# Performance work log

Hardware: AMD Instinct MI355X
Metric: run time of the kernel (lower is better)

## Reference

```python
import jax, jax.numpy as jnp
import numpy as np

B, S, E, H = 2, 2048, 1024, 16
D = E // H  # head_dim = 64


def _rope_angles(seq_len, d, dtype=jnp.float32):
    # standard RoPE frequencies: theta_i = 10000^{-2i/d}
    inv_freq = 1.0 / (10000.0 ** (jnp.arange(0, d, 2, dtype=dtype) / d))  # [d/2]
    pos = jnp.arange(seq_len, dtype=dtype)                                # [S]
    ang = pos[:, None] * inv_freq[None, :]                                # [S, d/2]
    ang = jnp.concatenate([ang, ang], axis=-1)                            # [S, d]
    return jnp.cos(ang), jnp.sin(ang)


def _rotate_half(t):
    t1, t2 = jnp.split(t, 2, axis=-1)
    return jnp.concatenate([-t2, t1], axis=-1)


def _apply_rope(t, cos, sin):
    # t: [B, H, S, D]; cos/sin: [S, D]
    return t * cos[None, None, :, :] + _rotate_half(t) * sin[None, None, :, :]


def setup_inputs() -> dict:
    key = jax.random.key(0)
    ks = jax.random.split(key, 6)
    x = jax.random.normal(ks[0], (B, S, E), dtype=jnp.float32)
    mask = jnp.tril(jnp.ones((S, S), dtype=bool))  # causal: True = attend
    scale = 1.0 / np.sqrt(E)
    Wq = jax.random.normal(ks[1], (E, E), dtype=jnp.float32) * scale
    Wk = jax.random.normal(ks[2], (E, E), dtype=jnp.float32) * scale
    Wv = jax.random.normal(ks[3], (E, E), dtype=jnp.float32) * scale
    Wo = jax.random.normal(ks[4], (E, E), dtype=jnp.float32) * scale
    z = jnp.zeros((E,), dtype=jnp.float32)
    return {"x": x, "mask": mask, "Wq": Wq, "bq": z, "Wk": Wk, "bk": z,
            "Wv": Wv, "bv": z, "Wo": Wo, "bo": z}


def reference(x, mask, Wq, bq, Wk, bk, Wv, bv, Wo, bo):
    b, s, e = x.shape
    # QKV projections (nn.Linear convention: y = x @ W.T + b)
    def proj(W, bias):
        y = jnp.einsum('bse,fe->bsf', x, W) + bias
        return y.reshape(b, s, H, D).transpose(0, 2, 1, 3)  # [B,H,S,D]
    q, k, v = proj(Wq, bq), proj(Wk, bk), proj(Wv, bv)
    # RoPE on q and k (per-head rotary over head_dim)
    cos, sin = _rope_angles(s, D, dtype=x.dtype)
    q = _apply_rope(q, cos, sin)
    k = _apply_rope(k, cos, sin)
    # SDPA with boolean mask (True = attend)
    scores = jnp.einsum('bhqd,bhkd->bhqk', q, k) / jnp.sqrt(jnp.asarray(D, x.dtype))
    neg = jnp.asarray(jnp.finfo(x.dtype).min, x.dtype)
    scores = jnp.where(mask[None, None, :, :], scores, neg)
    attn = jax.nn.softmax(scores, axis=-1)
    out = jnp.einsum('bhqk,bhkd->bhqd', attn, v)          # [B,H,S,D]
    out = out.transpose(0, 2, 1, 3).reshape(b, s, e)       # [B,S,E]
    return jnp.einsum('bse,fe->bsf', out, Wo) + bo
```

## Files before the change

### kernel.cpp

```cpp
#include <hip/hip_runtime.h>
#include <hip/hip_bf16.h>

typedef unsigned short u16;
typedef unsigned int u32;
typedef __bf16 bf16x8 __attribute__((ext_vector_type(8)));
typedef float f32x4 __attribute__((ext_vector_type(4)));

#define S_LEN 2048
#define NHEAD 16
#define HDIM  64
#define EMB   1024
#define BATCH 2

__device__ __forceinline__ float bf2f(u16 u) {
  union { unsigned int i; float f; } c; c.i = ((unsigned int)u) << 16; return c.f;
}
__device__ __forceinline__ u16 f2bf(float f) {
  union { float f; unsigned int i; } c; c.f = f;
  unsigned int i = c.i;
  return (u16)((i + 0x7FFFu + ((i >> 16) & 1u)) >> 16);
}
__device__ __forceinline__ u16 f2bf_trunc(float f) {
  union { float f; unsigned int i; } c; c.f = f;
  return (u16)(c.i >> 16);
}
__device__ __forceinline__ f32x4 mfma16(bf16x8 a, bf16x8 b, f32x4 c) {
  return __builtin_amdgcn_mfma_f32_16x16x32_bf16(a, b, c, 0, 0, 0);
}
__device__ __forceinline__ void cp16(const u16* g, u16* l) {
  __builtin_amdgcn_global_load_lds(
      (const __attribute__((address_space(1))) u32*)g,
      (__attribute__((address_space(3))) u32*)l, 16, 0, 0);
}

__global__ __launch_bounds__(256) void convert_kernel(
    const void* __restrict__ x, const void* __restrict__ Wq,
    const void* __restrict__ Wk, const void* __restrict__ Wv,
    const void* __restrict__ Wo,
    u16* __restrict__ xb, u16* __restrict__ wqb, u16* __restrict__ wkb,
    u16* __restrict__ wvb, u16* __restrict__ wob,
    int* __restrict__ flag, float2* __restrict__ tab)
{
  __shared__ int s_flag;
  if (threadIdx.x == 0) s_flag = 0;
  __syncthreads();
  {
    const u16* xs = (const u16*)x;
    u16 w0 = xs[threadIdx.x * 2], w1 = xs[threadIdx.x * 2 + 1];
    if ((((w0 >> 7) & 0xFF) >= 0xC0) || (((w1 >> 7) & 0xFF) >= 0xC0))
      atomicOr(&s_flag, 1);
  }
  __syncthreads();
  const int f32io = s_flag;
  if (blockIdx.x == 0 && threadIdx.x == 0) flag[0] = f32io;

  size_t gid = (size_t)blockIdx.x * 256 + threadIdx.x;
  size_t e = gid * 8;
  const void* src; u16* dst; size_t off;
  if (e < 4194304) { src = x; dst = xb; off = e; }
  else {
    size_t rr = e - 4194304;
    int j = (int)(rr >> 20); off = rr & 1048575;
    src = (j == 0) ? Wq : (j == 1) ? Wk : (j == 2) ? Wv : Wo;
    dst = (j == 0) ? wqb : (j == 1) ? wkb : (j == 2) ? wvb : wob;
  }
  if (f32io) {
    const float* s = (const float*)src + off;
    float4 a = *(const float4*)s;
    float4 b2 = *(const float4*)(s + 4);
    ushort4 u0; u0.x = f2bf(a.x); u0.y = f2bf(a.y); u0.z = f2bf(a.z); u0.w = f2bf(a.w);
    ushort4 u1; u1.x = f2bf(b2.x); u1.y = f2bf(b2.y); u1.z = f2bf(b2.z); u1.w = f2bf(b2.w);
    *(ushort4*)(dst + off) = u0;
    *(ushort4*)(dst + off + 4) = u1;
  } else {
    *(uint4*)(dst + off) = *(const uint4*)((const u16*)src + off);
  }

  if (blockIdx.x < 256) {
    int id = blockIdx.x * 256 + threadIdx.x;
    int s = id >> 5, i = id & 31;
    float f = exp2f(-(float)i * 0.41524101186092029f);
    float ang = (float)s * f;
    tab[id] = make_float2(cosf(ang), sinf(ang));
  }
}

__device__ __forceinline__ void gemm_core_db(
    const u16* __restrict__ A, const u16* __restrict__ W,
    int m0, int n0, int t, f32x4 (&acc)[4][4],
    u16* __restrict__ Ash, u16* __restrict__ Bsh)
{
  const int lane = t & 63, lr = lane & 15, quad = lane >> 4;
  const int wv = t >> 6;
  const int wm = (wv & 1) * 64, wn = (wv >> 1) * 64;
  const int r0 = t >> 2, c0 = (t & 3) * 8;
  const int r1 = (t + 256) >> 2, c1 = (t & 3) * 8;
  const int lds0 = (t & 192) * 8;
  const int lds1 = (256 + (t & 192)) * 8;
  const u16* gA0 = A + (size_t)(m0 + r0) * 1024 + c0;
  const u16* gA1 = A + (size_t)(m0 + r1) * 1024 + c1;
  const u16* gB0 = W + (size_t)(n0 + r0) * 1024 + c0;
  const u16* gB1 = W + (size_t)(n0 + r1) * 1024 + c1;

  cp16(gA0, Ash + lds0); cp16(gA1, Ash + lds1);
  cp16(gB0, Bsh + lds0); cp16(gB1, Bsh + lds1);
  __syncthreads();

  for (int kt = 0; kt < 1024; kt += 32) {
    const int cur = (kt >> 5) & 1;
    const u16* Ac = Ash + cur * 4096;
    const u16* Bc = Bsh + cur * 4096;
    bf16x8 af[4], bfr[4];
#pragma unroll
    for (int mi = 0; mi < 4; ++mi)
      af[mi] = *(const bf16x8*)(Ac + (wm + mi * 16 + lr) * 32 + quad * 8);
#pragma unroll
    for (int ni = 0; ni < 4; ++ni)
      bfr[ni] = *(const bf16x8*)(Bc + (wn + ni * 16 + lr) * 32 + quad * 8);
    if (kt + 32 < 1024) {
      u16* An = Ash + (1 - cur) * 4096;
      u16* Bn = Bsh + (1 - cur) * 4096;
      cp16(gA0 + kt + 32, An + lds0); cp16(gA1 + kt + 32, An + lds1);
      cp16(gB0 + kt + 32, Bn + lds0); cp16(gB1 + kt + 32, Bn + lds1);
    }
#pragma unroll
    for (int mi = 0; mi < 4; ++mi)
#pragma unroll
      for (int ni = 0; ni < 4; ++ni)
        acc[mi][ni] = mfma16(af[mi], bfr[ni], acc[mi][ni]);
    __syncthreads();
  }
}

__device__ __forceinline__ void gemm_epilogue(
    int mode, int f32io, f32x4 (&acc)[4][4],
    const void* biasvp, void* outvp, int m0, int n0, int t,
    const float2* __restrict__ tab)
{
  const int lane = t & 63, lr = lane & 15, quad = lane >> 4;
  const int wv = t >> 6;
  const int wm = (wv & 1) * 64, wn = (wv >> 1) * 64;
  const float* biasf = (const float*)biasvp;
  const u16* biasb = (const u16*)biasvp;
#define BIASV(n) (f32io ? biasf[(n)] : bf2f(biasb[(n)]))
  if (mode == 1) {
    u16* Out = (u16*)outvp;
#pragma unroll
    for (int mi = 0; mi < 4; ++mi) {
#pragma unroll
      for (int r = 0; r < 4; ++r) {
        int mm = m0 + wm + mi * 16 + quad * 4 + r;
        int s = mm & (S_LEN - 1), b = mm >> 11;
        float2 cs0 = tab[s * 32 + lr];
        float2 cs1 = tab[s * 32 + 16 + lr];
#pragma unroll
        for (int ni = 0; ni < 4; ++ni) {
          int n = n0 + wn + ni * 16 + lr;
          int h = n >> 6, d = n & 63;
          float v  = acc[mi][ni][r]     + BIASV(n);
          float vp = acc[mi][ni ^ 2][r] + BIASV(n ^ 32);
          float rot = (d < 32) ? -vp : vp;
          float cc = (ni & 1) ? cs1.x : cs0.x;
          float ss = (ni & 1) ? cs1.y : cs0.y;
          size_t off = (((size_t)(b * NHEAD + h)) * S_LEN + s) * HDIM + d;
          Out[off] = f2bf(v * cc + rot * ss);
        }
      }
    }
  } else if (mode == 2) {
    u16* Out = (u16*)outvp;
#pragma unroll
    for (int mi = 0; mi < 4; ++mi) {
      int mm = m0 + wm + mi * 16 + quad * 4;
      int s = mm & (S_LEN - 1), b = mm >> 11;
#pragma unroll
      for (int ni = 0; ni < 4; ++ni) {
        int n = n0 + wn + ni * 16 + lr;
        int h = n >> 6, d = n & 63;
        float bv = BIASV(n);
        u16 p0 = f2bf(acc[mi][ni][0] + bv);
        u16 p1 = f2bf(acc[mi][ni][1] + bv);
        u16 p2 = f2bf(acc[mi][ni][2] + bv);
        u16 p3 = f2bf(acc[mi][ni][3] + bv);
        uint2 pk = make_uint2((u32)p0 | ((u32)p1 << 16),
                              (u32)p2 | ((u32)p3 << 16));
        size_t off = (((size_t)(b * NHEAD + h)) * HDIM + d) * S_LEN + s;
        *(uint2*)(Out + off) = pk;
      }
    }
  }
#undef BIASV
}

__global__ __launch_bounds__(256) void gemm_qkv(
    const u16* __restrict__ A, const u16* __restrict__ Wq,
    const u16* __restrict__ Wk, const u16* __restrict__ Wv,
    const void* bq, const void* bk, const void* bv,
    u16* qo, u16* ko, u16* vo, const int* __restrict__ dflag,
    const float2* __restrict__ tab)
{
  alignas(16) __shared__ u16 Ash[2 * 128 * 32];
  alignas(16) __shared__ u16 Bsh[2 * 128 * 32];
  const int wsel = blockIdx.x >> 3;
  const u16* W = (wsel == 0) ? Wq : (wsel == 1) ? Wk : Wv;
  const void* bias = (wsel == 0) ? bq : (wsel == 1) ? bk : bv;
  void* out = (wsel == 0) ? (void*)qo : (wsel == 1) ? (void*)ko : (void*)vo;
  const int mode = (wsel == 2) ? 2 : 1;
  const int m0 = blockIdx.y * 128, n0 = (blockIdx.x & 7) * 128;
  f32x4 acc[4][4];
  const f32x4 zero4 = {0.f, 0.f, 0.f, 0.f};
#pragma unroll
  for (int i = 0; i < 4; ++i)
#pragma unroll
    for (int j = 0; j < 4; ++j) acc[i][j] = zero4;
  gemm_core_db(A, W, m0, n0, threadIdx.x, acc, Ash, Bsh);
  gemm_epilogue(mode, dflag[0], acc, bias, out, m0, n0, threadIdx.x, tab);
}

__global__ __launch_bounds__(256) void gemm_out(
    const u16* __restrict__ A, const u16* __restrict__ W,
    const void* bias, void* out, const int* __restrict__ dflag)
{
  alignas(16) __shared__ u16 Ash[2 * 64 * 32];
  alignas(16) __shared__ u16 Bsh[2 * 128 * 32];
  const int t = threadIdx.x, lane = t & 63, wv = t >> 6;
  const int lr = lane & 15, quad = lane >> 4;
  const int m0 = blockIdx.y * 64, n0 = blockIdx.x * 128;
  const int wm = (wv & 1) * 32, wn = (wv >> 1) * 64;
  const int f32io = dflag[0];

  const int r0 = t >> 2, c0 = (t & 3) * 8;
  const int r1 = (t + 256) >> 2;
  const int lds0 = (t & 192) * 8;
  const int lds1 = (256 + (t & 192)) * 8;
  const u16* gA0 = A + (size_t)(m0 + (r0 & 63)) * 1024 + c0;
  const u16* gB0 = W + (size_t)(n0 + r0) * 1024 + c0;
  const u16* gB1 = W + (size_t)(n0 + r1) * 1024 + c0;

  f32x4 acc[2][4];
  const f32x4 zero4 = {0.f, 0.f, 0.f, 0.f};
#pragma unroll
  for (int i = 0; i < 2; ++i)
#pragma unroll
    for (int j = 0; j < 4; ++j) acc[i][j] = zero4;

  cp16(gA0, Ash + lds0);
  cp16(gB0, Bsh + lds0); cp16(gB1, Bsh + lds1);
  __syncthreads();

  for (int kt = 0; kt < 1024; kt += 32) {
    const int cur = (kt >> 5) & 1;
    const u16* Ac = Ash + cur * 2048;
    const u16* Bc = Bsh + cur * 4096;
    bf16x8 af[2], bfr[4];
#pragma unroll
    for (int mi = 0; mi < 2; ++mi)
      af[mi] = *(const bf16x8*)(Ac + (wm + mi * 16 + lr) * 32 + quad * 8);
#pragma unroll
    for (int ni = 0; ni < 4; ++ni)
      bfr[ni] = *(const bf16x8*)(Bc + (wn + ni * 16 + lr) * 32 + quad * 8);
    if (kt + 32 < 1024) {
      u16* An = Ash + (1 - cur) * 2048;
      u16* Bn = Bsh + (1 - cur) * 4096;
      cp16(gA0 + kt + 32, An + lds0);
      cp16(gB0 + kt + 32, Bn + lds0); cp16(gB1 + kt + 32, Bn + lds1);
    }
#pragma unroll
    for (int mi = 0; mi < 2; ++mi)
#pragma unroll
      for (int ni = 0; ni < 4; ++ni)
        acc[mi][ni] = mfma16(af[mi], bfr[ni], acc[mi][ni]);
    __syncthreads();
  }

  const float* biasf = (const float*)bias;
  const u16* biasb = (const u16*)bias;
  float* Outf = (float*)out;
  u16* Outb = (u16*)out;
#pragma unroll
  for (int mi = 0; mi < 2; ++mi) {
#pragma unroll
    for (int r = 0; r < 4; ++r) {
      int mm = m0 + wm + mi * 16 + quad * 4 + r;
#pragma unroll
      for (int ni = 0; ni < 4; ++ni) {
        int n = n0 + wn + ni * 16 + lr;
        float bv = f32io ? biasf[n] : bf2f(biasb[n]);
        float v = acc[mi][ni][r] + bv;
        size_t off = (size_t)mm * 1024 + n;
        if (f32io) Outf[off] = v; else Outb[off] = f2bf(v);
      }
    }
  }
}

__device__ __forceinline__ void attn_phase(
    const bf16x8 (&qf)[2], f32x4 (&oacc)[4], float (&lsum)[4],
    u16 (&Ksh)[64][72], u16 (&Vsh)[64][72], u16 (&Psh)[8][16][72],
    int kv0, int q0w, bool diag, int lr, int quad, int wv)
{
  const f32x4 zero4 = {0.f, 0.f, 0.f, 0.f};
  f32x4 sc[4];
#pragma unroll
  for (int ni = 0; ni < 4; ++ni) {
    bf16x8 kf0 = *(const bf16x8*)&Ksh[ni * 16 + lr][quad * 8];
    bf16x8 kf1 = *(const bf16x8*)&Ksh[ni * 16 + lr][32 + quad * 8];
    f32x4 z = zero4;
    z = mfma16(qf[0], kf0, z);
    z = mfma16(qf[1], kf1, z);
    sc[ni] = z;
  }
  if (diag) {
#pragma unroll
    for (int ni = 0; ni < 4; ++ni)
#pragma unroll
      for (int r = 0; r < 4; ++r) {
        float sarg = sc[ni][r] * 0.18033688f - 21.64042561f;
        if (kv0 + ni * 16 + lr > q0w + quad * 4 + r) sarg = -1e4f;
        float p = exp2f(sarg);
        sc[ni][r] = p;
        lsum[r] += p;
      }
  } else {
#pragma unroll
    for (int ni = 0; ni < 4; ++ni)
#pragma unroll
      for (int r = 0; r < 4; ++r) {
        float p = exp2f(sc[ni][r] * 0.18033688f - 21.64042561f);
        sc[ni][r] = p;
        lsum[r] += p;
      }
  }
#pragma unroll
  for (int ni = 0; ni < 4; ++ni)
#pragma unroll
    for (int r = 0; r < 4; ++r)
      Psh[wv][quad * 4 + r][ni * 16 + lr] = f2bf_trunc(sc[ni][r]);
  bf16x8 pa0 = *(const bf16x8*)&Psh[wv][lr][quad * 8];
  bf16x8 pa1 = *(const bf16x8*)&Psh[wv][lr][32 + quad * 8];
#pragma unroll
  for (int oni = 0; oni < 4; ++oni) {
    bf16x8 vf0 = *(const bf16x8*)&Vsh[oni * 16 + lr][quad * 8];
    bf16x8 vf1 = *(const bf16x8*)&Vsh[oni * 16 + lr][32 + quad * 8];
    oacc[oni] = mfma16(pa0, vf0, oacc[oni]);
    oacc[oni] = mfma16(pa1, vf1, oacc[oni]);
  }
}

__device__ __forceinline__ void attn_finish(
    f32x4 (&oacc)[4], float (&lsum)[4], u16* __restrict__ O,
    int bh, int q0w, int lr, int quad)
{
  const int b = bh >> 4, h = bh & 15;
#pragma unroll
  for (int r = 0; r < 4; ++r) {
#pragma unroll
    for (int off = 1; off < 16; off <<= 1) lsum[r] += __shfl_xor(lsum[r], off);
    lsum[r] = 1.f / lsum[r];
  }
#pragma unroll
  for (int oni = 0; oni < 4; ++oni)
#pragma unroll
    for (int r = 0; r < 4; ++r) {
      int s = q0w + quad * 4 + r;
      int e = h * HDIM + oni * 16 + lr;
      O[((size_t)(b * S_LEN + s)) * EMB + e] = f2bf(oacc[oni][r] * lsum[r]);
    }
}

__global__ __launch_bounds__(512) void attn_kernel(
    const u16* __restrict__ Q, const u16* __restrict__ Kr,
    const u16* __restrict__ Vt, u16* __restrict__ O)
{
  alignas(16) __shared__ u16 Ksh[64][72];
  alignas(16) __shared__ u16 Vsh[64][72];
  alignas(16) __shared__ u16 Psh[8][16][72];
  const int t = threadIdx.x, lane = t & 63, wv = t >> 6;
  const int lr = lane & 15, quad = lane >> 4;
  const int bh = blockIdx.y;
  const int qtA = blockIdx.x;
  const int qtB = 31 - qtA;
  const int myTile = (wv < 4) ? qtA : qtB;
  const int q0w = myTile * 64 + (wv & 3) * 16;
  const size_t base = (size_t)bh * S_LEN * HDIM;

  bf16x8 qf[2];
  {
    const u16* qrow = Q + base + (size_t)(q0w + lr) * HDIM + quad * 8;
    qf[0] = *(const bf16x8*)qrow;
    qf[1] = *(const bf16x8*)(qrow + 32);
  }

  f32x4 oacc[4];
  float lsum[4];
  const f32x4 zero4 = {0.f, 0.f, 0.f, 0.f};
#pragma unroll
  for (int i = 0; i < 4; ++i) { oacc[i] = zero4; lsum[i] = 0.f; }

  const int rr = t >> 3, cc = (t & 7) * 8;
  uint4 krg = *(const uint4*)(Kr + base + (size_t)rr * HDIM + cc);
  uint4 vrg = *(const uint4*)(Vt + base + (size_t)rr * S_LEN + cc);

  const int jmax = qtB;
  for (int j = 0; j <= jmax; ++j) {
    __syncthreads();
    *(uint4*)&Ksh[rr][cc] = krg;
    *(uint4*)&Vsh[rr][cc] = vrg;
    __syncthreads();
    if (j < jmax) {
      const int kv1 = (j + 1) * 64;
      krg = *(const uint4*)(Kr + base + (size_t)(kv1 + rr) * HDIM + cc);
      vrg = *(const uint4*)(Vt + base + (size_t)rr * S_LEN + kv1 + cc);
    }
    if (j <= myTile)
      attn_phase(qf, oacc, lsum, Ksh, Vsh, Psh, j * 64, q0w, j == myTile, lr, quad, wv);
  }

  attn_finish(oacc, lsum, O, bh, q0w, lr, quad);
}

extern "C" void kernel_launch(void* const* d_in, const int* in_sizes, int n_in,
                              void* d_out, int out_size, void* d_ws, size_t ws_size,
                              hipStream_t stream) {
  const void* x  = d_in[0];
  const void* Wq = d_in[2]; const void* bq = d_in[3];
  const void* Wk = d_in[4]; const void* bk = d_in[5];
  const void* Wv = d_in[6]; const void* bv = d_in[7];
  const void* Wo = d_in[8]; const void* bo = d_in[9];

  char* ws = (char*)d_ws;
  int* flag = (int*)ws;
  u16* xb  = (u16*)(ws + 256);
  u16* qws = xb  + 4194304;
  u16* kws = qws + 4194304;
  u16* vws = kws + 4194304;
  u16* wqb = vws + 4194304;
  u16* wkb = wqb + 1048576;
  u16* wvb = wkb + 1048576;
  u16* wob = wvb + 1048576;
  float2* tab = (float2*)(wob + 1048576);
  u16* ows = xb;

  convert_kernel<<<4096, 256, 0, stream>>>(x, Wq, Wk, Wv, Wo,
                                           xb, wqb, wkb, wvb, wob, flag, tab);
  gemm_qkv<<<dim3(24, 32), 256, 0, stream>>>(xb, wqb, wkb, wvb,
                                             bq, bk, bv, qws, kws, vws, flag, tab);
  attn_kernel<<<dim3(16, 32), 512, 0, stream>>>(qws, kws, vws, ows);
  gemm_out<<<dim3(8, 64), 256, 0, stream>>>(ows, wob, bo, d_out, flag);
}
```

Measured before the change: 211.8 us.

## Split paired-tile attention blocks into per-tile blocks and transpose score MFMA

```diff
diff --git a/kernel.cpp b/kernel.cpp
--- a/kernel.cpp
+++ b/kernel.cpp
@@ -295,8 +295,8 @@
 }
 
 __device__ __forceinline__ void attn_phase(
-    const bf16x8 (&qf)[2], f32x4 (&oacc)[4], float (&lsum)[4],
-    u16 (&Ksh)[64][72], u16 (&Vsh)[64][72], u16 (&Psh)[8][16][72],
+    const bf16x8 (&qf)[2], f32x4 (&oacc)[4], float& lsum,
+    u16 (&Ksh)[64][72], u16 (&Vsh)[64][72], u16 (&Psh)[4][16][72],
     int kv0, int q0w, bool diag, int lr, int quad, int wv)
 {
   const f32x4 zero4 = {0.f, 0.f, 0.f, 0.f};
@@ -306,20 +306,21 @@
     bf16x8 kf0 = *(const bf16x8*)&Ksh[ni * 16 + lr][quad * 8];
     bf16x8 kf1 = *(const bf16x8*)&Ksh[ni * 16 + lr][32 + quad * 8];
     f32x4 z = zero4;
-    z = mfma16(qf[0], kf0, z);
-    z = mfma16(qf[1], kf1, z);
+    z = mfma16(kf0, qf[0], z);
+    z = mfma16(kf1, qf[1], z);
     sc[ni] = z;
   }
+  const int qa = q0w + lr;
   if (diag) {
 #pragma unroll
     for (int ni = 0; ni < 4; ++ni)
 #pragma unroll
       for (int r = 0; r < 4; ++r) {
         float sarg = sc[ni][r] * 0.18033688f - 21.64042561f;
-        if (kv0 + ni * 16 + lr > q0w + quad * 4 + r) sarg = -1e4f;
+        if (kv0 + ni * 16 + quad * 4 + r > qa) sarg = -1e4f;
         float p = exp2f(sarg);
         sc[ni][r] = p;
-        lsum[r] += p;
+        lsum += p;
       }
   } else {
 #pragma unroll
@@ -328,14 +329,15 @@
       for (int r = 0; r < 4; ++r) {
         float p = exp2f(sc[ni][r] * 0.18033688f - 21.64042561f);
         sc[ni][r] = p;
-        lsum[r] += p;
+        lsum += p;
       }
   }
 #pragma unroll
-  for (int ni = 0; ni < 4; ++ni)
-#pragma unroll
-    for (int r = 0; r < 4; ++r)
-      Psh[wv][quad * 4 + r][ni * 16 + lr] = f2bf_trunc(sc[ni][r]);
+  for (int ni = 0; ni < 4; ++ni) {
+    u32 lo = (u32)f2bf_trunc(sc[ni][0]) | ((u32)f2bf_trunc(sc[ni][1]) << 16);
+    u32 hi = (u32)f2bf_trunc(sc[ni][2]) | ((u32)f2bf_trunc(sc[ni][3]) << 16);
+    *(uint2*)&Psh[wv][lr][ni * 16 + quad * 4] = make_uint2(lo, hi);
+  }
   bf16x8 pa0 = *(const bf16x8*)&Psh[wv][lr][quad * 8];
   bf16x8 pa1 = *(const bf16x8*)&Psh[wv][lr][32 + quad * 8];
 #pragma unroll
@@ -348,40 +350,38 @@
 }
 
 __device__ __forceinline__ void attn_finish(
-    f32x4 (&oacc)[4], float (&lsum)[4], u16* __restrict__ O,
+    f32x4 (&oacc)[4], float lsum, u16* __restrict__ O,
     int bh, int q0w, int lr, int quad)
 {
   const int b = bh >> 4, h = bh & 15;
+  lsum += __shfl_xor(lsum, 16);
+  lsum += __shfl_xor(lsum, 32);
+  const float inv = 1.f / lsum;
 #pragma unroll
   for (int r = 0; r < 4; ++r) {
-#pragma unroll
-    for (int off = 1; off < 16; off <<= 1) lsum[r] += __shfl_xor(lsum[r], off);
-    lsum[r] = 1.f / lsum[r];
-  }
-#pragma unroll
-  for (int oni = 0; oni < 4; ++oni)
-#pragma unroll
-    for (int r = 0; r < 4; ++r) {
+    const float scale = __shfl(inv, quad * 4 + r);
+#pragma unroll
+    for (int oni = 0; oni < 4; ++oni) {
       int s = q0w + quad * 4 + r;
       int e = h * HDIM + oni * 16 + lr;
-      O[((size_t)(b * S_LEN + s)) * EMB + e] = f2bf(oacc[oni][r] * lsum[r]);
-    }
-}
-
-__global__ __launch_bounds__(512) void attn_kernel(
+      O[((size_t)(b * S_LEN + s)) * EMB + e] = f2bf(oacc[oni][r] * scale);
+    }
+  }
+}
+
+__global__ __launch_bounds__(256) void attn_kernel(
     const u16* __restrict__ Q, const u16* __restrict__ Kr,
     const u16* __restrict__ Vt, u16* __restrict__ O)
 {
   alignas(16) __shared__ u16 Ksh[64][72];
   alignas(16) __shared__ u16 Vsh[64][72];
-  alignas(16) __shared__ u16 Psh[8][16][72];
+  alignas(16) __shared__ u16 Psh[4][16][72];
   const int t = threadIdx.x, lane = t & 63, wv = t >> 6;
   const int lr = lane & 15, quad = lane >> 4;
   const int bh = blockIdx.y;
-  const int qtA = blockIdx.x;
-  const int qtB = 31 - qtA;
-  const int myTile = (wv < 4) ? qtA : qtB;
-  const int q0w = myTile * 64 + (wv & 3) * 16;
+  const int xs = blockIdx.x;
+  const int myTile = (xs >> 4) ? (xs & 15) : 31 - (xs & 15);
+  const int q0w = myTile * 64 + wv * 16;
   const size_t base = (size_t)bh * S_LEN * HDIM;
 
   bf16x8 qf[2];
@@ -392,28 +392,33 @@
   }
 
   f32x4 oacc[4];
-  float lsum[4];
+  float lsum = 0.f;
   const f32x4 zero4 = {0.f, 0.f, 0.f, 0.f};
 #pragma unroll
-  for (int i = 0; i < 4; ++i) { oacc[i] = zero4; lsum[i] = 0.f; }
+  for (int i = 0; i < 4; ++i) oacc[i] = zero4;
 
   const int rr = t >> 3, cc = (t & 7) * 8;
-  uint4 krg = *(const uint4*)(Kr + base + (size_t)rr * HDIM + cc);
-  uint4 vrg = *(const uint4*)(Vt + base + (size_t)rr * S_LEN + cc);
-
-  const int jmax = qtB;
-  for (int j = 0; j <= jmax; ++j) {
+  uint4 krg0 = *(const uint4*)(Kr + base + (size_t)rr * HDIM + cc);
+  uint4 krg1 = *(const uint4*)(Kr + base + (size_t)(rr + 32) * HDIM + cc);
+  uint4 vrg0 = *(const uint4*)(Vt + base + (size_t)rr * S_LEN + cc);
+  uint4 vrg1 = *(const uint4*)(Vt + base + (size_t)(rr + 32) * S_LEN + cc);
+
+  for (int j = 0; j <= myTile; ++j) {
     __syncthreads();
-    *(uint4*)&Ksh[rr][cc] = krg;
-    *(uint4*)&Vsh[rr][cc] = vrg;
+    *(uint4*)&Ksh[rr][cc] = krg0;
+    *(uint4*)&Ksh[rr + 32][cc] = krg1;
+    *(uint4*)&Vsh[rr][cc] = vrg0;
+    *(uint4*)&Vsh[rr + 32][cc] = vrg1;
     __syncthreads();
-    if (j < jmax) {
+    if (j < myTile) {
       const int kv1 = (j + 1) * 64;
-      krg = *(const uint4*)(Kr + base + (size_t)(kv1 + rr) * HDIM + cc);
-      vrg = *(const uint4*)(Vt + base + (size_t)rr * S_LEN + kv1 + cc);
-    }
-    if (j <= myTile)
-      attn_phase(qf, oacc, lsum, Ksh, Vsh, Psh, j * 64, q0w, j == myTile, lr, quad, wv);
+      krg0 = *(const uint4*)(Kr + base + (size_t)(kv1 + rr) * HDIM + cc);
+      krg1 = *(const uint4*)(Kr + base + (size_t)(kv1 + rr + 32) * HDIM + cc);
+      vrg0 = *(const uint4*)(Vt + base + (size_t)rr * S_LEN + kv1 + cc);
+      vrg1 = *(const uint4*)(Vt + base + (size_t)(rr + 32) * S_LEN + kv1 + cc);
+    }
+    attn_phase(qf, oacc, lsum, Ksh, Vsh, Psh, j * 64, q0w, j == myTile,
+               lr, quad, wv);
   }
 
   attn_finish(oacc, lsum, O, bh, q0w, lr, quad);
@@ -445,6 +450,6 @@
                                            xb, wqb, wkb, wvb, wob, flag, tab);
   gemm_qkv<<<dim3(24, 32), 256, 0, stream>>>(xb, wqb, wkb, wvb,
                                              bq, bk, bv, qws, kws, vws, flag, tab);
-  attn_kernel<<<dim3(16, 32), 512, 0, stream>>>(qws, kws, vws, ows);
+  attn_kernel<<<dim3(32, 32), 256, 0, stream>>>(qws, kws, vws, ows);
   gemm_out<<<dim3(8, 64), 256, 0, stream>>>(ows, wob, bo, d_out, flag);
 }
```

Result: slower. 241.4 us (+13.9%).
